# Kernel tuning notes

Hardware: AMD Instinct MI355X
Metric: run time of the kernel (lower is better)

## Reference

```python
import jax, jax.numpy as jnp
import numpy as np

B, T, D = 2, 1024, 2048
N, K, H = 16, 4, 128          # num_heads, num_kv_heads, head_dim
TC = 1024                     # cached tokens
S = TC + T
MAX_WAVELENGTH = 10000.0
BIG_NEG = -2.3819763e38


def _apply_rope(x, positions):
    """RoPE: positions [B,L] applied to x [B,L,heads,H]."""
    half = x.shape[-1] // 2
    freq_exponents = (2.0 / x.shape[-1]) * jnp.arange(half, dtype=jnp.float32)
    timescale = MAX_WAVELENGTH ** freq_exponents                      # [H/2]
    radians = (positions.astype(jnp.float32)[..., None] / timescale)[..., None, :]  # [B,L,1,H/2]
    sin, cos = jnp.sin(radians), jnp.cos(radians)
    x1, x2 = jnp.split(x, 2, axis=-1)
    res = jnp.concatenate([x1 * cos - x2 * sin, x2 * cos + x1 * sin], axis=-1)
    return res.astype(x.dtype)


def setup_inputs() -> dict:
    key = jax.random.key(0)
    ks = jax.random.split(key, 8)
    x = jax.random.normal(ks[0], (B, T, D), dtype=jnp.float32)
    # new tokens sit right after the cache
    positions = jnp.broadcast_to(TC + jnp.arange(T, dtype=jnp.int32), (B, T))
    # causal mask over [cache + new]: query t may attend to keys s <= TC + t
    s_idx = jnp.arange(S)[None, :]
    t_idx = jnp.arange(T)[:, None]
    attn_mask = jnp.broadcast_to((s_idx <= TC + t_idx)[None, None, :, :], (B, 1, T, S))
    cache_k = jax.random.normal(ks[1], (B, TC, K, H), dtype=jnp.float32)
    cache_v = jax.random.normal(ks[2], (B, TC, K, H), dtype=jnp.float32)
    # lecun-normal-ish fan-in scaling (fan_in = D for projections, N*H for output)
    w_q = jax.random.normal(ks[3], (N, D, H), dtype=jnp.float32) * (D ** -0.5)
    w_kv = jax.random.normal(ks[4], (2, K, D, H), dtype=jnp.float32) * (D ** -0.5)
    w_out = jax.random.normal(ks[5], (N, H, D), dtype=jnp.float32) * ((N * H) ** -0.5)
    return {"x": x, "positions": positions, "attn_mask": attn_mask,
            "cache_k": cache_k, "cache_v": cache_v,
            "w_q": w_q, "w_kv": w_kv, "w_out": w_out}


def reference(x, positions, attn_mask, cache_k, cache_v, w_q, w_kv, w_out):
    dtype = x.dtype
    # projections (GQA path: num_kv_heads != num_heads)
    q = jnp.einsum('BTD,NDH->BTNH', x, w_q.astype(dtype))
    kv = jnp.einsum('BSD,CKDH->CBSKH', x, w_kv.astype(dtype))
    k_new, v_new = kv[0], kv[1]
    # inline RoPE + query scaling
    q = _apply_rope(q, positions) * (H ** -0.5)
    k_new = _apply_rope(k_new, positions)
    # KV-cache concat
    k = jnp.concatenate([cache_k, k_new], axis=1)   # [B,S,K,H]
    v = jnp.concatenate([cache_v, v_new], axis=1)
    # group heads: B T (K G) H -> B T K G H
    G = N // K
    qg = q.reshape(q.shape[0], q.shape[1], K, G, H)
    logits = jnp.einsum('BTKGH,BSKH->BKGTS', qg, k,
                        preferred_element_type=jnp.float32)
    masked = jnp.where(attn_mask[:, :, None, :, :], logits, BIG_NEG)
    probs = jax.nn.softmax(masked, axis=-1).astype(dtype)
    enc = jnp.einsum('BKGTS,BSKH->BTKGH', probs, v)
    enc = enc.reshape(enc.shape[0], enc.shape[1], N, H)  # B T (K G) H
    out = jnp.einsum('BTNH,NHD->BTD', enc, w_out.astype(dtype))
    return out, k, v
```

## Files before the change

kernel.cpp:

```cpp
#include <hip/hip_runtime.h>

#define B_  2
#define T_  1024
#define D_  2048
#define NH  16
#define KH  4
#define HD  128
#define TC_ 1024
#define S_  2048

typedef __bf16 bf16x4v __attribute__((ext_vector_type(4)));
typedef __bf16 bf16x8v __attribute__((ext_vector_type(8)));
typedef float  f32x4v  __attribute__((ext_vector_type(4)));

__device__ __forceinline__ void async_copy16(void* lds, const void* g) {
    __builtin_amdgcn_global_load_lds(
        (__attribute__((address_space(1))) void*)g,
        (__attribute__((address_space(3))) void*)lds, 16, 0, 0);
}

__global__ void cvt_x(const float* __restrict__ x, __bf16* __restrict__ xb) {
    int i = (blockIdx.x * 256 + threadIdx.x) * 4;
    float4 v = *(const float4*)(x + i);
    bf16x4v o; o[0]=(__bf16)v.x; o[1]=(__bf16)v.y; o[2]=(__bf16)v.z; o[3]=(__bf16)v.w;
    *(bf16x4v*)(xb + i) = o;
}

__global__ void tp_w(const float* __restrict__ in, __bf16* __restrict__ out) {
    __shared__ float tile[32][33];
    int h0 = blockIdx.x * 32;
    int d0 = blockIdx.y * 32;
    const float* ip = in + (size_t)blockIdx.z * (D_ * HD);
    __bf16* op = out + (size_t)blockIdx.z * (D_ * HD);
    int tx = threadIdx.x, ty = threadIdx.y;
    for (int i = 0; i < 32; i += 8)
        tile[ty + i][tx] = ip[(size_t)(d0 + ty + i) * HD + h0 + tx];
    __syncthreads();
    for (int i = 0; i < 32; i += 8)
        op[(size_t)(h0 + ty + i) * D_ + d0 + tx] = (__bf16)tile[tx][ty + i];
}

__global__ void tp_wout(const float* __restrict__ in, __bf16* __restrict__ out) {
    __shared__ float tile[32][33];
    int d0 = blockIdx.x * 32;
    int h0 = blockIdx.y * 32;
    int n  = blockIdx.z;
    const float* ip = in + (size_t)n * (HD * D_);
    int tx = threadIdx.x, ty = threadIdx.y;
    for (int i = 0; i < 32; i += 8)
        tile[ty + i][tx] = ip[(size_t)(h0 + ty + i) * D_ + d0 + tx];
    __syncthreads();
    for (int i = 0; i < 32; i += 8)
        out[(size_t)(d0 + ty + i) * (NH * HD) + n * HD + h0 + tx] = (__bf16)tile[tx][ty + i];
}

__global__ void tp_v(const float* __restrict__ vout, __bf16* __restrict__ vtb) {
    __shared__ float tile[32][33];
    int z = blockIdx.z; int b = z / KH, kh = z % KH;
    int h0 = blockIdx.x * 32;
    int s0 = blockIdx.y * 32;
    const float* ip = vout + ((size_t)b * S_ * KH + kh) * HD;
    int tx = threadIdx.x, ty = threadIdx.y;
    for (int i = 0; i < 32; i += 8)
        tile[ty + i][tx] = ip[(size_t)(s0 + ty + i) * (KH * HD) + h0 + tx];
    __syncthreads();
    __bf16* op = vtb + ((size_t)b * KH + kh) * (size_t)HD * S_;
    for (int i = 0; i < 32; i += 8)
        op[(size_t)(h0 + ty + i) * S_ + s0 + tx] = (__bf16)tile[tx][ty + i];
}

__global__ void copy_cache(const float4* __restrict__ ck, const float4* __restrict__ cv,
                           float* __restrict__ kout, float* __restrict__ vout,
                           __bf16* __restrict__ kb) {
    int i = blockIdx.x * 256 + threadIdx.x;
    int b = i >> 17;
    int r = i & 131071;
    float4 kv = ck[i];
    ((float4*)(kout + (size_t)b * S_ * KH * HD))[r] = kv;
    ((float4*)(vout + (size_t)b * S_ * KH * HD))[r] = cv[i];
    int h4 = r & 31;
    int kh = (r >> 5) & 3;
    int s  = r >> 7;
    bf16x4v o; o[0]=(__bf16)kv.x; o[1]=(__bf16)kv.y; o[2]=(__bf16)kv.z; o[3]=(__bf16)kv.w;
    *(bf16x4v*)(kb + (((size_t)(b * KH + kh) * S_ + s) * HD) + h4 * 4) = o;
}

__global__ __launch_bounds__(256, 2)
void gemm_bt(const __bf16* __restrict__ A, const __bf16* __restrict__ BT,
             float* __restrict__ C, int ldc) {
    __shared__ __bf16 As[128 * 64];
    __shared__ __bf16 Bs[128 * 64];
    const int m0 = blockIdx.x * 128, n0 = blockIdx.y * 128;
    const int tid = threadIdx.x;
    const int wave = tid >> 6, lane = tid & 63;
    const int quad = lane >> 4, l16 = lane & 15;
    const int wm = (wave & 1) * 64, wn = (wave >> 1) * 64;
    const int lrow = lane >> 3;
    const int lsw  = (lane & 7) ^ (lrow & 7);

    f32x4v acc[4][4];
    for (int i = 0; i < 4; i++)
        for (int j = 0; j < 4; j++)
            acc[i][j] = (f32x4v){0.f, 0.f, 0.f, 0.f};

    const __bf16* Abase = A + (size_t)m0 * D_;
    const __bf16* Bbase = BT + (size_t)n0 * D_;

    for (int k0 = 0; k0 < D_; k0 += 64) {
        for (int j = 0; j < 4; j++) {
            int r = wave * 32 + j * 8;
            async_copy16(As + (size_t)r * 64,
                         Abase + (size_t)(r + lrow) * D_ + k0 + lsw * 8);
            async_copy16(Bs + (size_t)r * 64,
                         Bbase + (size_t)(r + lrow) * D_ + k0 + lsw * 8);
        }
        __syncthreads();
        for (int ks = 0; ks < 2; ks++) {
            const int ch = ((ks * 4 + quad) ^ (l16 & 7)) * 8;
            bf16x8v a[4], b[4];
            for (int i = 0; i < 4; i++)
                a[i] = *(const bf16x8v*)(As + (wm + i * 16 + l16) * 64 + ch);
            for (int j = 0; j < 4; j++)
                b[j] = *(const bf16x8v*)(Bs + (wn + j * 16 + l16) * 64 + ch);
            for (int i = 0; i < 4; i++)
                for (int j = 0; j < 4; j++)
                    acc[i][j] = __builtin_amdgcn_mfma_f32_16x16x32_bf16(a[i], b[j], acc[i][j], 0, 0, 0);
        }
        __syncthreads();
    }
    for (int i = 0; i < 4; i++)
        for (int j = 0; j < 4; j++)
            for (int r = 0; r < 4; r++) {
                int row = m0 + wm + i * 16 + quad * 4 + r;
                int col = n0 + wn + j * 16 + l16;
                C[(size_t)row * ldc + col] = acc[i][j][r];
            }
}

__global__ void finish_rope(const float* __restrict__ proj, const int* __restrict__ pos,
                            __bf16* __restrict__ qws, float* __restrict__ kout,
                            float* __restrict__ vout, __bf16* __restrict__ kb) {
    const int tau = blockIdx.x;
    const int b = tau >> 10, t = tau & 1023;
    const float p = (float)pos[tau];
    const float* pr = proj + (size_t)tau * 3072;
    const float qscale = 0.08838834764831845f;
    for (int idx = threadIdx.x; idx < (NH + KH) * 64; idx += 256) {
        int head = idx >> 6;
        int hh = idx & 63;
        float ang = p * __expf(-(float)hh * (9.210340371976184f / 64.0f));
        float sn, cs;
        __sincosf(ang, &sn, &cs);
        if (head < NH) {
            float x1 = pr[head * HD + hh], x2 = pr[head * HD + hh + 64];
            size_t qo = ((size_t)tau * NH + head) * HD;
            qws[qo + hh]      = (__bf16)((x1 * cs - x2 * sn) * qscale);
            qws[qo + hh + 64] = (__bf16)((x2 * cs + x1 * sn) * qscale);
        } else {
            int kh = head - NH;
            float x1 = pr[2048 + kh * HD + hh], x2 = pr[2048 + kh * HD + hh + 64];
            float k1 = x1 * cs - x2 * sn, k2 = x2 * cs + x1 * sn;
            size_t ko = ((size_t)(b * S_ + TC_ + t) * KH + kh) * HD;
            kout[ko + hh]      = k1;
            kout[ko + hh + 64] = k2;
            size_t kbo = ((size_t)(b * KH + kh) * S_ + TC_ + t) * HD;
            kb[kbo + hh]      = (__bf16)k1;
            kb[kbo + hh + 64] = (__bf16)k2;
        }
    }
    for (int idx = threadIdx.x; idx < KH * HD; idx += 256) {
        int kh = idx >> 7, h = idx & 127;
        vout[((size_t)(b * S_ + TC_ + t) * KH + kh) * HD + h] = pr[2560 + kh * HD + h];
    }
}

__global__ __launch_bounds__(512, 1)
void attn(const __bf16* __restrict__ qws, const __bf16* __restrict__ kb,
          const __bf16* __restrict__ vtb, __bf16* __restrict__ enc) {
    __shared__ __bf16 Qs[128 * 128];
    __shared__ __bf16 Ks[2][64 * 128];
    __shared__ __bf16 Vs[2][128 * 64];
    __shared__ __bf16 Ps[128 * 64];

    const int t0 = blockIdx.x * 128;
    const int n  = blockIdx.y;
    const int b  = blockIdx.z;
    const int kh = n / (NH / KH);
    const int tid = threadIdx.x, wave = tid >> 6, lane = tid & 63;
    const int quad = lane >> 4, l16 = lane & 15;
    const int wm = wave * 16;

    const __bf16* kbase = kb  + ((size_t)(b * KH + kh)) * S_ * HD;
    const __bf16* vbase = vtb + ((size_t)(b * KH + kh)) * (size_t)HD * S_;

    {
        const __bf16* qtile = qws + ((size_t)(b * T_ + t0) * NH + n) * HD;
        for (int jj = 0; jj < 4; jj++) {
            int r0 = wm + jj * 4;
            int row = r0 + (lane >> 4);
            async_copy16(Qs + (size_t)r0 * 128,
                         qtile + (size_t)row * (NH * HD) + (((lane & 15) ^ (row & 15)) * 8));
        }
    }

    auto stageK = [&](int buf, int s0) {
        const __bf16* ktile = kbase + (size_t)s0 * HD;
        for (int jj = 0; jj < 2; jj++) {
            int r0 = wave * 8 + jj * 4;
            int row = r0 + (lane >> 4);
            async_copy16(&Ks[buf][(size_t)r0 * 128],
                         ktile + (size_t)row * HD + (((lane & 15) ^ (row & 15)) * 8));
        }
    };
    auto stageV = [&](int buf, int s0) {
        const __bf16* vtile = vbase + s0;
        for (int jj = 0; jj < 2; jj++) {
            int r0 = wave * 16 + jj * 8;
            int row = r0 + (lane >> 3);
            async_copy16(&Vs[buf][(size_t)r0 * 64],
                         vtile + (size_t)row * S_ + (((lane & 7) ^ (row & 7)) * 8));
        }
    };

    float m_run[4], l_run[4];
    f32x4v o_acc[8];
    for (int r = 0; r < 4; r++) { m_run[r] = -INFINITY; l_run[r] = 0.f; }
    for (int j = 0; j < 8; j++) o_acc[j] = (f32x4v){0.f, 0.f, 0.f, 0.f};

    const int nS = (TC_ + t0 + 128) >> 6;

    stageK(0, 0);
    stageV(0, 0);
    __syncthreads();

    int cur = 0;
    for (int st = 0; st < nS; st++) {
        const int s0 = st * 64;

        if (st + 1 < nS) {
            stageK(cur ^ 1, s0 + 64);
            stageV(cur ^ 1, s0 + 64);
        }

        f32x4v sc[4];
        for (int j = 0; j < 4; j++) sc[j] = (f32x4v){0.f, 0.f, 0.f, 0.f};
        for (int ks = 0; ks < 4; ks++) {
            int ch = ((ks * 4 + quad) ^ l16) * 8;
            bf16x8v a = *(const bf16x8v*)(Qs + (wm + l16) * 128 + ch);
            bf16x8v bb[4];
            for (int j = 0; j < 4; j++)
                bb[j] = *(const bf16x8v*)(&Ks[cur][(j * 16 + l16) * 128 + ch]);
            for (int j = 0; j < 4; j++)
                sc[j] = __builtin_amdgcn_mfma_f32_16x16x32_bf16(a, bb[j], sc[j], 0, 0, 0);
        }

        if (st >= nS - 2) {
            int off = s0 - (TC_ + t0);
            for (int j = 0; j < 4; j++)
                for (int r = 0; r < 4; r++) {
                    int row = wm + quad * 4 + r;
                    int col = j * 16 + l16;
                    if (off + col > row) sc[j][r] = -3.0e38f;
                }
        }

        for (int r = 0; r < 4; r++) {
            float mx = sc[0][r];
            for (int j = 1; j < 4; j++) mx = fmaxf(mx, sc[j][r]);
            for (int off = 8; off >= 1; off >>= 1) mx = fmaxf(mx, __shfl_xor(mx, off, 64));
            mx = fmaxf(mx, m_run[r]);
            float alpha = __expf(m_run[r] - mx);
            m_run[r] = mx;
            float s = 0.f;
            for (int j = 0; j < 4; j++) {
                float pv = __expf(sc[j][r] - mx);
                sc[j][r] = pv;
                s += pv;
            }
            for (int off = 8; off >= 1; off >>= 1) s += __shfl_xor(s, off, 64);
            l_run[r] = l_run[r] * alpha + s;
            for (int j = 0; j < 8; j++) o_acc[j][r] *= alpha;
        }

        for (int j = 0; j < 4; j++)
            for (int r = 0; r < 4; r++) {
                int row = wm + quad * 4 + r;
                int c = (j * 2 + (l16 >> 3)) ^ (row & 7);
                Ps[row * 64 + c * 8 + (l16 & 7)] = (__bf16)sc[j][r];
            }

        asm volatile("s_waitcnt lgkmcnt(0)" ::: "memory");
        __builtin_amdgcn_s_barrier();
        asm volatile("" ::: "memory");
        __builtin_amdgcn_sched_barrier(0);

        for (int ks = 0; ks < 2; ks++) {
            int ch = ((ks * 4 + quad) ^ (l16 & 7)) * 8;
            bf16x8v a = *(const bf16x8v*)(Ps + (wm + l16) * 64 + ch);
            bf16x8v bb[8];
            for (int j = 0; j < 8; j++)
                bb[j] = *(const bf16x8v*)(&Vs[cur][(j * 16 + l16) * 64 + ch]);
            for (int j = 0; j < 8; j++)
                o_acc[j] = __builtin_amdgcn_mfma_f32_16x16x32_bf16(a, bb[j], o_acc[j], 0, 0, 0);
        }

        __syncthreads();
        cur ^= 1;
    }

    for (int r = 0; r < 4; r++) {
        float inv = 1.0f / l_run[r];
        int row = wm + quad * 4 + r;
        for (int j = 0; j < 8; j++) {
            int col = j * 16 + l16;
            enc[((size_t)(b * T_ + t0 + row) * NH + n) * HD + col] =
                (__bf16)(o_acc[j][r] * inv);
        }
    }
}

extern "C" void kernel_launch(void* const* d_in, const int* in_sizes, int n_in,
                              void* d_out, int out_size, void* d_ws, size_t ws_size,
                              hipStream_t stream) {
    const float* x       = (const float*)d_in[0];
    const int*   pos     = (const int*)d_in[1];
    const float* cache_k = (const float*)d_in[3];
    const float* cache_v = (const float*)d_in[4];
    const float* w_q     = (const float*)d_in[5];
    const float* w_kv    = (const float*)d_in[6];
    const float* w_out   = (const float*)d_in[7];

    float* out  = (float*)d_out;
    float* kout = out  + (size_t)B_ * T_ * D_;
    float* vout = kout + (size_t)B_ * S_ * KH * HD;

    char* ws = (char*)d_ws;
    __bf16* xb   = (__bf16*)ws;  ws += (size_t)B_ * T_ * D_ * 2;
    __bf16* wt   = (__bf16*)ws;  ws += (size_t)3072 * D_ * 2;
    __bf16* wot  = (__bf16*)ws;  ws += (size_t)D_ * NH * HD * 2;
    float*  proj = (float*)ws;   ws += (size_t)B_ * T_ * 3072 * 4;
    __bf16* qws  = (__bf16*)ws;  ws += (size_t)B_ * T_ * NH * HD * 2;
    __bf16* kbuf = (__bf16*)ws;  ws += (size_t)B_ * S_ * KH * HD * 2;
    __bf16* vtb  = (__bf16*)ws;  ws += (size_t)B_ * S_ * KH * HD * 2;
    __bf16* enc  = (__bf16*)ws;

    cvt_x<<<4096, 256, 0, stream>>>(x, xb);
    tp_w<<<dim3(4, 64, 16), dim3(32, 8), 0, stream>>>(w_q, wt);
    tp_w<<<dim3(4, 64, 8),  dim3(32, 8), 0, stream>>>(w_kv, wt + (size_t)16 * HD * D_);
    tp_wout<<<dim3(64, 4, 16), dim3(32, 8), 0, stream>>>(w_out, wot);
    copy_cache<<<1024, 256, 0, stream>>>((const float4*)cache_k, (const float4*)cache_v, kout, vout, kbuf);
    gemm_bt<<<dim3(16, 24), 256, 0, stream>>>(xb, wt, proj, 3072);
    finish_rope<<<2048, 256, 0, stream>>>(proj, pos, qws, kout, vout, kbuf);
    tp_v<<<dim3(4, 64, 8), dim3(32, 8), 0, stream>>>(vout, vtb);
    attn<<<dim3(8, 16, 2), 512, 0, stream>>>(qws, kbuf, vtb, enc);
    gemm_bt<<<dim3(16, 16), 256, 0, stream>>>(enc, wot, out, 2048);
}
```

Baseline: 295.2 us.

## Halve attention query tile, hold Q in registers, raise occupancy with setprio

```diff
diff --git a/kernel.cpp b/kernel.cpp
--- a/kernel.cpp
+++ b/kernel.cpp
@@ -174,15 +174,14 @@
     }
 }
 
-__global__ __launch_bounds__(512, 1)
+__global__ __launch_bounds__(256, 2)
 void attn(const __bf16* __restrict__ qws, const __bf16* __restrict__ kb,
           const __bf16* __restrict__ vtb, __bf16* __restrict__ enc) {
-    __shared__ __bf16 Qs[128 * 128];
     __shared__ __bf16 Ks[2][64 * 128];
     __shared__ __bf16 Vs[2][128 * 64];
-    __shared__ __bf16 Ps[128 * 64];
-
-    const int t0 = blockIdx.x * 128;
+    __shared__ __bf16 Ps[64 * 64];
+
+    const int t0 = blockIdx.x * 64;
     const int n  = blockIdx.y;
     const int b  = blockIdx.z;
     const int kh = n / (NH / KH);
@@ -193,31 +192,29 @@
     const __bf16* kbase = kb  + ((size_t)(b * KH + kh)) * S_ * HD;
     const __bf16* vbase = vtb + ((size_t)(b * KH + kh)) * (size_t)HD * S_;
 
+    bf16x8v qreg[4];
     {
-        const __bf16* qtile = qws + ((size_t)(b * T_ + t0) * NH + n) * HD;
+        const __bf16* qrow = qws + ((size_t)(b * T_ + t0 + wm + l16) * NH + n) * HD;
+#pragma unroll
+        for (int ks = 0; ks < 4; ks++)
+            qreg[ks] = *(const bf16x8v*)(qrow + (ks * 4 + quad) * 8);
+    }
+
+    auto stageK = [&](int bf, int s0) {
+        const __bf16* ktile = kbase + (size_t)s0 * HD;
         for (int jj = 0; jj < 4; jj++) {
-            int r0 = wm + jj * 4;
+            int r0 = wave * 16 + jj * 4;
             int row = r0 + (lane >> 4);
-            async_copy16(Qs + (size_t)r0 * 128,
-                         qtile + (size_t)row * (NH * HD) + (((lane & 15) ^ (row & 15)) * 8));
-        }
-    }
-
-    auto stageK = [&](int buf, int s0) {
-        const __bf16* ktile = kbase + (size_t)s0 * HD;
-        for (int jj = 0; jj < 2; jj++) {
-            int r0 = wave * 8 + jj * 4;
-            int row = r0 + (lane >> 4);
-            async_copy16(&Ks[buf][(size_t)r0 * 128],
+            async_copy16(&Ks[bf][(size_t)r0 * 128],
                          ktile + (size_t)row * HD + (((lane & 15) ^ (row & 15)) * 8));
         }
     };
-    auto stageV = [&](int buf, int s0) {
+    auto stageV = [&](int bf, int s0) {
         const __bf16* vtile = vbase + s0;
-        for (int jj = 0; jj < 2; jj++) {
-            int r0 = wave * 16 + jj * 8;
+        for (int jj = 0; jj < 4; jj++) {
+            int r0 = wave * 32 + jj * 8;
             int row = r0 + (lane >> 3);
-            async_copy16(&Vs[buf][(size_t)r0 * 64],
+            async_copy16(&Vs[bf][(size_t)r0 * 64],
                          vtile + (size_t)row * S_ + (((lane & 7) ^ (row & 7)) * 8));
         }
     };
@@ -227,7 +224,7 @@
     for (int r = 0; r < 4; r++) { m_run[r] = -INFINITY; l_run[r] = 0.f; }
     for (int j = 0; j < 8; j++) o_acc[j] = (f32x4v){0.f, 0.f, 0.f, 0.f};
 
-    const int nS = (TC_ + t0 + 128) >> 6;
+    const int nS = (TC_ + t0 + 64) >> 6;
 
     stageK(0, 0);
     stageV(0, 0);
@@ -235,32 +232,31 @@
 
     int cur = 0;
     for (int st = 0; st < nS; st++) {
-        const int s0 = st * 64;
-
         if (st + 1 < nS) {
-            stageK(cur ^ 1, s0 + 64);
-            stageV(cur ^ 1, s0 + 64);
+            stageK(cur ^ 1, (st + 1) * 64);
+            stageV(cur ^ 1, (st + 1) * 64);
         }
 
         f32x4v sc[4];
         for (int j = 0; j < 4; j++) sc[j] = (f32x4v){0.f, 0.f, 0.f, 0.f};
+        __builtin_amdgcn_s_setprio(1);
+#pragma unroll
         for (int ks = 0; ks < 4; ks++) {
-            int ch = ((ks * 4 + quad) ^ l16) * 8;
-            bf16x8v a = *(const bf16x8v*)(Qs + (wm + l16) * 128 + ch);
+            int ch = (ks * 4 + quad) ^ l16;
             bf16x8v bb[4];
             for (int j = 0; j < 4; j++)
-                bb[j] = *(const bf16x8v*)(&Ks[cur][(j * 16 + l16) * 128 + ch]);
+                bb[j] = *(const bf16x8v*)(&Ks[cur][(j * 16 + l16) * 128 + ch * 8]);
             for (int j = 0; j < 4; j++)
-                sc[j] = __builtin_amdgcn_mfma_f32_16x16x32_bf16(a, bb[j], sc[j], 0, 0, 0);
-        }
-
-        if (st >= nS - 2) {
-            int off = s0 - (TC_ + t0);
+                sc[j] = __builtin_amdgcn_mfma_f32_16x16x32_bf16(qreg[ks], bb[j], sc[j], 0, 0, 0);
+        }
+        __builtin_amdgcn_s_setprio(0);
+
+        if (st == nS - 1) {
             for (int j = 0; j < 4; j++)
                 for (int r = 0; r < 4; r++) {
                     int row = wm + quad * 4 + r;
                     int col = j * 16 + l16;
-                    if (off + col > row) sc[j][r] = -3.0e38f;
+                    if (col > row) sc[j][r] = -3.0e38f;
                 }
         }
 
@@ -291,18 +287,20 @@
 
         asm volatile("s_waitcnt lgkmcnt(0)" ::: "memory");
         __builtin_amdgcn_s_barrier();
-        asm volatile("" ::: "memory");
         __builtin_amdgcn_sched_barrier(0);
 
+        __builtin_amdgcn_s_setprio(1);
+#pragma unroll
         for (int ks = 0; ks < 2; ks++) {
-            int ch = ((ks * 4 + quad) ^ (l16 & 7)) * 8;
-            bf16x8v a = *(const bf16x8v*)(Ps + (wm + l16) * 64 + ch);
+            int ch = (ks * 4 + quad) ^ (l16 & 7);
+            bf16x8v a = *(const bf16x8v*)(Ps + (wm + l16) * 64 + ch * 8);
             bf16x8v bb[8];
             for (int j = 0; j < 8; j++)
-                bb[j] = *(const bf16x8v*)(&Vs[cur][(j * 16 + l16) * 64 + ch]);
+                bb[j] = *(const bf16x8v*)(&Vs[cur][(j * 16 + l16) * 64 + ch * 8]);
             for (int j = 0; j < 8; j++)
                 o_acc[j] = __builtin_amdgcn_mfma_f32_16x16x32_bf16(a, bb[j], o_acc[j], 0, 0, 0);
         }
+        __builtin_amdgcn_s_setprio(0);
 
         __syncthreads();
         cur ^= 1;
@@ -352,6 +350,6 @@
     gemm_bt<<<dim3(16, 24), 256, 0, stream>>>(xb, wt, proj, 3072);
     finish_rope<<<2048, 256, 0, stream>>>(proj, pos, qws, kout, vout, kbuf);
     tp_v<<<dim3(4, 64, 8), dim3(32, 8), 0, stream>>>(vout, vtb);
-    attn<<<dim3(8, 16, 2), 512, 0, stream>>>(qws, kbuf, vtb, enc);
+    attn<<<dim3(16, 16, 2), 256, 0, stream>>>(qws, kbuf, vtb, enc);
     gemm_bt<<<dim3(16, 16), 256, 0, stream>>>(enc, wot, out, 2048);
 }
```

After: 296.5 us. Within noise of the previous version (+0.4%).
